# Performance work log

Hardware: AMD Instinct MI355X
Metric: run time of the kernel (lower is better)

## Reference

```python
import jax, jax.numpy as jnp
import numpy as np

D_MODEL = 1024
NUM_HEADS = 16
HEAD_DIM = D_MODEL // NUM_HEADS


def setup_inputs() -> dict:
    key = jax.random.key(0)
    ks = jax.random.split(key, 9)
    B, S = 4, 2048
    s = 1.0 / np.sqrt(D_MODEL)
    return {
        "x": jax.random.normal(ks[0], (B, S, D_MODEL), dtype=jnp.float32),
        "Wq": jax.random.normal(ks[1], (D_MODEL, D_MODEL), dtype=jnp.float32) * s,
        "bq": jnp.zeros((D_MODEL,), dtype=jnp.float32),
        "Wk": jax.random.normal(ks[2], (D_MODEL, HEAD_DIM), dtype=jnp.float32) * s,
        "bk": jnp.zeros((HEAD_DIM,), dtype=jnp.float32),
        "Wv": jax.random.normal(ks[3], (D_MODEL, HEAD_DIM), dtype=jnp.float32) * s,
        "bv": jnp.zeros((HEAD_DIM,), dtype=jnp.float32),
        "Wo": jax.random.normal(ks[4], (D_MODEL, D_MODEL), dtype=jnp.float32) * s,
        "bo": jnp.zeros((D_MODEL,), dtype=jnp.float32),
    }


def reference(x, Wq, bq, Wk, bk, Wv, bv, Wo, bo):
    B, S, _ = x.shape
    H, Dh = NUM_HEADS, HEAD_DIM
    # projections
    Q = (x @ Wq + bq).reshape(B, S, H, Dh).transpose(0, 2, 1, 3)  # [B,H,S,Dh]
    K = x @ Wk + bk  # [B,S,Dh] (single shared KV head)
    V = x @ Wv + bv  # [B,S,Dh]
    # scores: Q @ K^T, broadcasting the single K head over all query heads
    A = jnp.einsum("bhqd,bkd->bhqk", Q, K)  # [B,H,S,S]
    causal = jnp.tril(jnp.ones((S, S), dtype=bool))
    A = jnp.where(causal, A, -jnp.inf)
    # original divides AFTER masking; -inf stays -inf so math is identical
    P = jax.nn.softmax(A / np.sqrt(Dh).astype(np.float32), axis=-1)
    O = jnp.einsum("bhqk,bkd->bhqd", P, V)  # [B,H,S,Dh]
    O = O.transpose(0, 2, 1, 3).reshape(B, S, H * Dh)
    return O @ Wo + bo
```

## Files before the change

kernel.cpp:

```cpp
#include <hip/hip_runtime.h>
#include <hip/hip_bf16.h>

typedef __bf16 bf16_t;
typedef __bf16 bf16x4 __attribute__((ext_vector_type(4)));
typedef __bf16 bf16x8 __attribute__((ext_vector_type(8)));
typedef float f32x4 __attribute__((ext_vector_type(4)));

#define AS1(p) ((const __attribute__((address_space(1))) void*)(p))
#define AS3(p) ((__attribute__((address_space(3))) void*)(p))

__device__ __forceinline__ f32x4 mfma16(bf16x8 a, bf16x8 b, f32x4 c) {
  return __builtin_amdgcn_mfma_f32_16x16x32_bf16(a, b, c, 0, 0, 0);
}

__global__ void cvt_f32_to_bf16(const float* __restrict__ in, bf16_t* __restrict__ out, int n) {
  int i = (blockIdx.x * 256 + threadIdx.x) * 4;
  if (i >= n) return;
  float4 v = *(const float4*)(in + i);
  bf16x4 o = {(bf16_t)v.x, (bf16_t)v.y, (bf16_t)v.z, (bf16_t)v.w};
  *(bf16x4*)(out + i) = o;
}

__global__ void transpose_cvt_t(const float* __restrict__ W, bf16_t* __restrict__ Wt,
                                int K, int N) {
  __shared__ float t[64][65];
  const int n0 = blockIdx.x * 64, k0 = blockIdx.y * 64;
  const int tx = threadIdx.x & 63, ty = threadIdx.x >> 6;
#pragma unroll
  for (int i = 0; i < 16; ++i)
    t[ty * 16 + i][tx] = W[(size_t)(k0 + ty * 16 + i) * N + n0 + tx];
  __syncthreads();
#pragma unroll
  for (int i = 0; i < 16; ++i)
    Wt[(size_t)(n0 + ty * 16 + i) * K + k0 + tx] = (bf16_t)t[tx][ty * 16 + i];
}

__global__ void transpose_v(const bf16_t* __restrict__ Vb, bf16_t* __restrict__ VtG) {
  __shared__ bf16_t t[64][72];
  const int s0 = blockIdx.x * 64, b = blockIdx.y;
  const int tx = threadIdx.x & 63, ty = threadIdx.x >> 6;
#pragma unroll
  for (int i = 0; i < 16; ++i)
    t[ty * 16 + i][tx] = Vb[(size_t)(b * 2048 + s0 + ty * 16 + i) * 64 + tx];
  __syncthreads();
#pragma unroll
  for (int i = 0; i < 16; ++i)
    VtG[(size_t)(b * 64 + ty * 16 + i) * 2048 + s0 + tx] = t[tx][ty * 16 + i];
}

__global__ __launch_bounds__(256, 2)
void gemm_nt_bias_b16(const bf16_t* __restrict__ A, const bf16_t* __restrict__ Bt,
                      const float* __restrict__ bias, bf16_t* __restrict__ C,
                      int M, int N, int K) {
  __shared__ __align__(16) bf16_t As[128 * 32];
  __shared__ __align__(16) bf16_t Bs[128 * 32];
  const int tid = threadIdx.x;
  const int w = tid >> 6, l = tid & 63;
  const int l15 = l & 15, q = l >> 4;
  const int m0 = blockIdx.x * 128, n0 = blockIdx.y * 128;
  const int mw = (w >> 1) * 64, nw = (w & 1) * 64;
  f32x4 acc[4][4] = {};
  const int kb = (l & 3) * 8;
  int rA[2], rB[2];
#pragma unroll
  for (int i = 0; i < 2; ++i) {
    int row = (i * 4 + w) * 16 + (l >> 2);
    rA[i] = m0 + row;
    int rb = n0 + row; if (rb >= N) rb = N - 1;
    rB[i] = rb;
  }
  for (int k0 = 0; k0 < K; k0 += 32) {
#pragma unroll
    for (int i = 0; i < 2; ++i) {
      int sg = i * 4 + w;
      __builtin_amdgcn_global_load_lds(AS1(A + (size_t)rA[i] * K + k0 + kb),
                                       AS3(As + sg * 512), 16, 0, 0);
      __builtin_amdgcn_global_load_lds(AS1(Bt + (size_t)rB[i] * K + k0 + kb),
                                       AS3(Bs + sg * 512), 16, 0, 0);
    }
    __syncthreads();
    bf16x8 af[4], bfr[4];
#pragma unroll
    for (int mi = 0; mi < 4; ++mi)
      af[mi] = *(const bf16x8*)(As + (mw + mi * 16 + l15) * 32 + q * 8);
#pragma unroll
    for (int ni = 0; ni < 4; ++ni)
      bfr[ni] = *(const bf16x8*)(Bs + (nw + ni * 16 + l15) * 32 + q * 8);
#pragma unroll
    for (int mi = 0; mi < 4; ++mi)
#pragma unroll
      for (int ni = 0; ni < 4; ++ni)
        acc[mi][ni] = mfma16(af[mi], bfr[ni], acc[mi][ni]);
    __syncthreads();
  }
#pragma unroll
  for (int ni = 0; ni < 4; ++ni) {
    int col = n0 + nw + ni * 16 + l15;
    if (col >= N) continue;
    float bv = bias[col];
#pragma unroll
    for (int mi = 0; mi < 4; ++mi)
#pragma unroll
      for (int r = 0; r < 4; ++r) {
        int row = m0 + mw + mi * 16 + q * 4 + r;
        C[(size_t)row * N + col] = (bf16_t)(acc[mi][ni][r] + bv);
      }
  }
}

__global__ __launch_bounds__(256, 2)
void gemm_nt_bias_f32(const bf16_t* __restrict__ A, const bf16_t* __restrict__ Bt,
                      const float* __restrict__ bias, float* __restrict__ C,
                      int M, int N, int K) {
  __shared__ __align__(16) bf16_t As[128 * 32];
  __shared__ __align__(16) bf16_t Bs[128 * 32];
  const int tid = threadIdx.x;
  const int w = tid >> 6, l = tid & 63;
  const int l15 = l & 15, q = l >> 4;
  const int m0 = blockIdx.x * 128, n0 = blockIdx.y * 128;
  const int mw = (w >> 1) * 64, nw = (w & 1) * 64;
  f32x4 acc[4][4] = {};
  const int kb = (l & 3) * 8;
  int rA[2], rB[2];
#pragma unroll
  for (int i = 0; i < 2; ++i) {
    int row = (i * 4 + w) * 16 + (l >> 2);
    rA[i] = m0 + row;
    int rb = n0 + row; if (rb >= N) rb = N - 1;
    rB[i] = rb;
  }
  for (int k0 = 0; k0 < K; k0 += 32) {
#pragma unroll
    for (int i = 0; i < 2; ++i) {
      int sg = i * 4 + w;
      __builtin_amdgcn_global_load_lds(AS1(A + (size_t)rA[i] * K + k0 + kb),
                                       AS3(As + sg * 512), 16, 0, 0);
      __builtin_amdgcn_global_load_lds(AS1(Bt + (size_t)rB[i] * K + k0 + kb),
                                       AS3(Bs + sg * 512), 16, 0, 0);
    }
    __syncthreads();
    bf16x8 af[4], bfr[4];
#pragma unroll
    for (int mi = 0; mi < 4; ++mi)
      af[mi] = *(const bf16x8*)(As + (mw + mi * 16 + l15) * 32 + q * 8);
#pragma unroll
    for (int ni = 0; ni < 4; ++ni)
      bfr[ni] = *(const bf16x8*)(Bs + (nw + ni * 16 + l15) * 32 + q * 8);
#pragma unroll
    for (int mi = 0; mi < 4; ++mi)
#pragma unroll
      for (int ni = 0; ni < 4; ++ni)
        acc[mi][ni] = mfma16(af[mi], bfr[ni], acc[mi][ni]);
    __syncthreads();
  }
#pragma unroll
  for (int ni = 0; ni < 4; ++ni) {
    int col = n0 + nw + ni * 16 + l15;
    if (col >= N) continue;
    float bv = bias[col];
#pragma unroll
    for (int mi = 0; mi < 4; ++mi)
#pragma unroll
      for (int r = 0; r < 4; ++r) {
        int row = m0 + mw + mi * 16 + q * 4 + r;
        C[(size_t)row * N + col] = acc[mi][ni][r] + bv;
      }
  }
}

__device__ __forceinline__ void attn_range(
    const bf16_t* __restrict__ Qb, const bf16_t* __restrict__ kbase,
    const bf16_t* __restrict__ vbase, int b, int h, int qt, int kt0, int kt1,
    int l15, int q, bf16_t* __restrict__ ps, f32x4 (&o)[4][4], float (&rs)[4]) {
  bf16x8 qf0[4], qf1[4];
#pragma unroll
  for (int nq = 0; nq < 4; ++nq) {
    const bf16_t* qp = Qb + (size_t)(b * 2048 + qt * 64 + nq * 16 + l15) * 1024 + h * 64 + q * 8;
    qf0[nq] = *(const bf16x8*)qp;
    qf1[nq] = *(const bf16x8*)(qp + 32);
  }
  const float c1 = 0.18033688f;
  for (int kt = kt0; kt < kt1; ++kt) {
    const bf16_t* kb = kbase + (size_t)kt * 64 * 64;
    bf16x8 ka0[4], ka1[4];
#pragma unroll
    for (int mk = 0; mk < 4; ++mk) {
      const bf16_t* kr = kb + (mk * 16 + l15) * 64;
      ka0[mk] = *(const bf16x8*)(kr + q * 8);
      ka1[mk] = *(const bf16x8*)(kr + 32 + q * 8);
    }
    bf16x8 va0[4], va1[4];
#pragma unroll
    for (int md = 0; md < 4; ++md) {
      const bf16_t* vr = vbase + (size_t)(md * 16 + l15) * 2048 + kt * 64;
      va0[md] = *(const bf16x8*)(vr + q * 8);
      va1[md] = *(const bf16x8*)(vr + 32 + q * 8);
    }
    const bool diag = (kt == qt);
#pragma unroll
    for (int mh = 0; mh < 2; ++mh) {
      f32x4 s2[2][4];
      __builtin_amdgcn_s_setprio(1);
#pragma unroll
      for (int mk2 = 0; mk2 < 2; ++mk2)
#pragma unroll
        for (int nq = 0; nq < 4; ++nq) {
          f32x4 t = {0.f, 0.f, 0.f, 0.f};
          t = mfma16(ka0[mh * 2 + mk2], qf0[nq], t);
          t = mfma16(ka1[mh * 2 + mk2], qf1[nq], t);
          s2[mk2][nq] = t;
        }
      __builtin_amdgcn_s_setprio(0);
#pragma unroll
      for (int nq = 0; nq < 4; ++nq)
#pragma unroll
        for (int mk2 = 0; mk2 < 2; ++mk2) {
          const int mk = mh * 2 + mk2;
          bf16x4 pk;
#pragma unroll
          for (int r = 0; r < 4; ++r) {
            float pv = __builtin_amdgcn_exp2f(s2[mk2][nq][r] * c1 - 16.0f);
            if (diag && (mk * 16 + q * 4 + r) > (nq * 16 + l15)) pv = 0.f;
            rs[nq] += pv;
            pk[r] = (bf16_t)pv;
          }
          *(bf16x4*)(ps + nq * 1152 + l15 * 72 + mk * 16 + q * 4) = pk;
        }
    }
#pragma unroll
    for (int nq = 0; nq < 4; ++nq) {
      bf16x8 pb0 = *(const bf16x8*)(ps + nq * 1152 + l15 * 72 + q * 8);
      bf16x8 pb1 = *(const bf16x8*)(ps + nq * 1152 + l15 * 72 + 32 + q * 8);
      __builtin_amdgcn_s_setprio(1);
#pragma unroll
      for (int md = 0; md < 4; ++md) {
        o[md][nq] = mfma16(va0[md], pb0, o[md][nq]);
        o[md][nq] = mfma16(va1[md], pb1, o[md][nq]);
      }
      __builtin_amdgcn_s_setprio(0);
    }
  }
}

__device__ __forceinline__ void attn_finalize(bf16_t* __restrict__ AO, int b, int h,
                                              int qt, int l15, int q,
                                              f32x4 (&o)[4][4], float (&rs)[4]) {
#pragma unroll
  for (int nq = 0; nq < 4; ++nq) {
    rs[nq] += __shfl_xor(rs[nq], 16);
    rs[nq] += __shfl_xor(rs[nq], 32);
  }
  float inv[4];
#pragma unroll
  for (int nq = 0; nq < 4; ++nq) inv[nq] = 1.f / rs[nq];
#pragma unroll
  for (int md = 0; md < 4; ++md)
#pragma unroll
    for (int nq = 0; nq < 4; ++nq) {
      bf16x4 ov = {(bf16_t)(o[md][nq][0] * inv[nq]), (bf16_t)(o[md][nq][1] * inv[nq]),
                   (bf16_t)(o[md][nq][2] * inv[nq]), (bf16_t)(o[md][nq][3] * inv[nq])};
      *(bf16x4*)(AO + (size_t)(b * 2048 + qt * 64 + nq * 16 + l15) * 1024 +
                 h * 64 + md * 16 + q * 4) = ov;
    }
}

__global__ __launch_bounds__(128, 2)
void mqa_attn6(const bf16_t* __restrict__ Qb, const bf16_t* __restrict__ Kb,
               const bf16_t* __restrict__ VtG, bf16_t* __restrict__ AO) {
  __shared__ __align__(16) bf16_t Ps[2][4][16 * 72];
  __shared__ __align__(16) float Oc[4096];
  __shared__ float RSc[256];
  const int u = blockIdx.x;
  const int b = u & 3;
  const int h = (u >> 2) & 15;
  const int p = (u >> 6) & 15;
  const int w = threadIdx.x >> 6, l = threadIdx.x & 63;
  const int l15 = l & 15, q = l >> 4;
  const int qt_h = 31 - p;
  bf16_t* ps = &Ps[w][0][0];
  const bf16_t* kbase = Kb + (size_t)b * 2048 * 64;
  const bf16_t* vbase = VtG + (size_t)b * 64 * 2048;

  f32x4 o[4][4] = {};
  float rs[4] = {0.f, 0.f, 0.f, 0.f};

  if (w == 0) {
    attn_range(Qb, kbase, vbase, b, h, qt_h, 0, 17, l15, q, ps, o, rs);
    __syncthreads();
#pragma unroll
    for (int md = 0; md < 4; ++md)
#pragma unroll
      for (int nq = 0; nq < 4; ++nq)
        o[md][nq] += *(const f32x4*)&Oc[((md * 4 + nq) * 64 + l) * 4];
#pragma unroll
    for (int nq = 0; nq < 4; ++nq) rs[nq] += RSc[l * 4 + nq];
    attn_finalize(AO, b, h, qt_h, l15, q, o, rs);
  } else {
    attn_range(Qb, kbase, vbase, b, h, p, 0, p + 1, l15, q, ps, o, rs);
    attn_finalize(AO, b, h, p, l15, q, o, rs);
#pragma unroll
    for (int md = 0; md < 4; ++md)
#pragma unroll
      for (int nq = 0; nq < 4; ++nq) o[md][nq] = f32x4{0.f, 0.f, 0.f, 0.f};
    rs[0] = rs[1] = rs[2] = rs[3] = 0.f;
    attn_range(Qb, kbase, vbase, b, h, qt_h, 17, 32 - p, l15, q, ps, o, rs);
#pragma unroll
    for (int md = 0; md < 4; ++md)
#pragma unroll
      for (int nq = 0; nq < 4; ++nq)
        *(f32x4*)&Oc[((md * 4 + nq) * 64 + l) * 4] = o[md][nq];
#pragma unroll
    for (int nq = 0; nq < 4; ++nq) RSc[l * 4 + nq] = rs[nq];
    __syncthreads();
  }
}

extern "C" void kernel_launch(void* const* d_in, const int* in_sizes, int n_in,
                              void* d_out, int out_size, void* d_ws, size_t ws_size,
                              hipStream_t stream) {
  (void)in_sizes; (void)n_in; (void)out_size; (void)ws_size;
  const int BS = 8192;
  const float* x  = (const float*)d_in[0];
  const float* Wq = (const float*)d_in[1];
  const float* bq = (const float*)d_in[2];
  const float* Wk = (const float*)d_in[3];
  const float* bk = (const float*)d_in[4];
  const float* Wv = (const float*)d_in[5];
  const float* bv = (const float*)d_in[6];
  const float* Wo = (const float*)d_in[7];
  const float* bo = (const float*)d_in[8];
  float* out = (float*)d_out;

  bf16_t* p = (bf16_t*)d_ws;
  bf16_t* WqT = p; p += 1024 * 1024;
  bf16_t* WkT = p; p += 64 * 1024;
  bf16_t* WvT = p; p += 64 * 1024;
  bf16_t* WoT = p; p += 1024 * 1024;
  bf16_t* xb  = p; p += (size_t)BS * 1024;
  bf16_t* Qb  = p; p += (size_t)BS * 1024;
  bf16_t* Kb  = p; p += (size_t)BS * 64;
  bf16_t* Vb  = p; p += (size_t)BS * 64;
  bf16_t* AO  = xb;
  bf16_t* VtG = WqT;

  cvt_f32_to_bf16<<<(BS * 1024 / 4 + 255) / 256, 256, 0, stream>>>(x, xb, BS * 1024);
  transpose_cvt_t<<<dim3(16, 16), 256, 0, stream>>>(Wq, WqT, 1024, 1024);
  transpose_cvt_t<<<dim3(1, 16), 256, 0, stream>>>(Wk, WkT, 1024, 64);
  transpose_cvt_t<<<dim3(1, 16), 256, 0, stream>>>(Wv, WvT, 1024, 64);
  transpose_cvt_t<<<dim3(16, 16), 256, 0, stream>>>(Wo, WoT, 1024, 1024);

  gemm_nt_bias_b16<<<dim3(BS / 128, 8), 256, 0, stream>>>(xb, WqT, bq, Qb, BS, 1024, 1024);
  gemm_nt_bias_b16<<<dim3(BS / 128, 1), 256, 0, stream>>>(xb, WkT, bk, Kb, BS, 64, 1024);
  gemm_nt_bias_b16<<<dim3(BS / 128, 1), 256, 0, stream>>>(xb, WvT, bv, Vb, BS, 64, 1024);

  transpose_v<<<dim3(32, 4), 256, 0, stream>>>(Vb, VtG);

  mqa_attn6<<<dim3(1024), 128, 0, stream>>>(Qb, Kb, VtG, AO);

  gemm_nt_bias_f32<<<dim3(BS / 128, 8), 256, 0, stream>>>(AO, WoT, bo, out, BS, 1024, 1024);
}
```

Measured before the change: 277.1 us.

## Fuse prep kernels, merge K/V GEMM with V transpose, template diagonal masking

Folds the x conversion, four weight transposes and a K/V bias concat into one prep launch. The separate K and V projections become a single N=128 GEMM that also writes V transposed directly, removing the transpose_v kernel. The attention loop is split into a templated step so only the diagonal tile pays for the causal mask check. The goal is fewer launches, less intermediate traffic and less per-tile branching, at the cost of scattered 2-byte transposed stores in the GEMM epilogue and a wider KV stride in the attention loads.

```diff
diff --git a/kernel.cpp b/kernel.cpp
--- a/kernel.cpp
+++ b/kernel.cpp
@@ -13,18 +13,32 @@
   return __builtin_amdgcn_mfma_f32_16x16x32_bf16(a, b, c, 0, 0, 0);
 }
 
-__global__ void cvt_f32_to_bf16(const float* __restrict__ in, bf16_t* __restrict__ out, int n) {
-  int i = (blockIdx.x * 256 + threadIdx.x) * 4;
-  if (i >= n) return;
-  float4 v = *(const float4*)(in + i);
-  bf16x4 o = {(bf16_t)v.x, (bf16_t)v.y, (bf16_t)v.z, (bf16_t)v.w};
-  *(bf16x4*)(out + i) = o;
-}
-
-__global__ void transpose_cvt_t(const float* __restrict__ W, bf16_t* __restrict__ Wt,
-                                int K, int N) {
+__global__ void prep(const float* __restrict__ x, const float* __restrict__ Wq,
+                     const float* __restrict__ Wk, const float* __restrict__ Wv,
+                     const float* __restrict__ Wo, const float* __restrict__ bk,
+                     const float* __restrict__ bv, bf16_t* __restrict__ xb,
+                     bf16_t* __restrict__ WqT, bf16_t* __restrict__ WkvT,
+                     bf16_t* __restrict__ WoT, float* __restrict__ bkv) {
+  const int u = blockIdx.x;
+  if (u >= 545) {
+    int i = ((u - 545) * 256 + threadIdx.x) * 4;
+    float4 v = *(const float4*)(x + i);
+    bf16x4 o = {(bf16_t)v.x, (bf16_t)v.y, (bf16_t)v.z, (bf16_t)v.w};
+    *(bf16x4*)(xb + i) = o;
+    return;
+  }
+  if (u == 544) {
+    if (threadIdx.x < 128)
+      bkv[threadIdx.x] = (threadIdx.x < 64) ? bk[threadIdx.x] : bv[threadIdx.x - 64];
+    return;
+  }
+  const float* W; bf16_t* Wt; int N, bx, by;
+  if (u < 256)      { W = Wq; Wt = WqT;             N = 1024; bx = u & 15;        by = u >> 4; }
+  else if (u < 272) { W = Wk; Wt = WkvT;            N = 64;   bx = 0;             by = u - 256; }
+  else if (u < 288) { W = Wv; Wt = WkvT + 64 * 1024; N = 64;  bx = 0;             by = u - 272; }
+  else              { W = Wo; Wt = WoT;             N = 1024; bx = (u - 288) & 15; by = (u - 288) >> 4; }
   __shared__ float t[64][65];
-  const int n0 = blockIdx.x * 64, k0 = blockIdx.y * 64;
+  const int n0 = bx * 64, k0 = by * 64;
   const int tx = threadIdx.x & 63, ty = threadIdx.x >> 6;
 #pragma unroll
   for (int i = 0; i < 16; ++i)
@@ -32,20 +46,7 @@
   __syncthreads();
 #pragma unroll
   for (int i = 0; i < 16; ++i)
-    Wt[(size_t)(n0 + ty * 16 + i) * K + k0 + tx] = (bf16_t)t[tx][ty * 16 + i];
-}
-
-__global__ void transpose_v(const bf16_t* __restrict__ Vb, bf16_t* __restrict__ VtG) {
-  __shared__ bf16_t t[64][72];
-  const int s0 = blockIdx.x * 64, b = blockIdx.y;
-  const int tx = threadIdx.x & 63, ty = threadIdx.x >> 6;
-#pragma unroll
-  for (int i = 0; i < 16; ++i)
-    t[ty * 16 + i][tx] = Vb[(size_t)(b * 2048 + s0 + ty * 16 + i) * 64 + tx];
-  __syncthreads();
-#pragma unroll
-  for (int i = 0; i < 16; ++i)
-    VtG[(size_t)(b * 64 + ty * 16 + i) * 2048 + s0 + tx] = t[tx][ty * 16 + i];
+    Wt[(size_t)(n0 + ty * 16 + i) * 1024 + k0 + tx] = (bf16_t)t[tx][ty * 16 + i];
 }
 
 __global__ __launch_bounds__(256, 2)
@@ -109,6 +110,67 @@
 }
 
 __global__ __launch_bounds__(256, 2)
+void gemm_kv(const bf16_t* __restrict__ A, const bf16_t* __restrict__ Bt,
+             const float* __restrict__ bias, bf16_t* __restrict__ C,
+             bf16_t* __restrict__ VtG, int M, int K) {
+  __shared__ __align__(16) bf16_t As[128 * 32];
+  __shared__ __align__(16) bf16_t Bs[128 * 32];
+  const int tid = threadIdx.x;
+  const int w = tid >> 6, l = tid & 63;
+  const int l15 = l & 15, q = l >> 4;
+  const int m0 = blockIdx.x * 128;
+  const int mw = (w >> 1) * 64, nw = (w & 1) * 64;
+  f32x4 acc[4][4] = {};
+  const int kb = (l & 3) * 8;
+  int rA[2], rB[2];
+#pragma unroll
+  for (int i = 0; i < 2; ++i) {
+    int row = (i * 4 + w) * 16 + (l >> 2);
+    rA[i] = m0 + row;
+    rB[i] = row;
+  }
+  for (int k0 = 0; k0 < K; k0 += 32) {
+#pragma unroll
+    for (int i = 0; i < 2; ++i) {
+      int sg = i * 4 + w;
+      __builtin_amdgcn_global_load_lds(AS1(A + (size_t)rA[i] * K + k0 + kb),
+                                       AS3(As + sg * 512), 16, 0, 0);
+      __builtin_amdgcn_global_load_lds(AS1(Bt + (size_t)rB[i] * K + k0 + kb),
+                                       AS3(Bs + sg * 512), 16, 0, 0);
+    }
+    __syncthreads();
+    bf16x8 af[4], bfr[4];
+#pragma unroll
+    for (int mi = 0; mi < 4; ++mi)
+      af[mi] = *(const bf16x8*)(As + (mw + mi * 16 + l15) * 32 + q * 8);
+#pragma unroll
+    for (int ni = 0; ni < 4; ++ni)
+      bfr[ni] = *(const bf16x8*)(Bs + (nw + ni * 16 + l15) * 32 + q * 8);
+#pragma unroll
+    for (int mi = 0; mi < 4; ++mi)
+#pragma unroll
+      for (int ni = 0; ni < 4; ++ni)
+        acc[mi][ni] = mfma16(af[mi], bfr[ni], acc[mi][ni]);
+    __syncthreads();
+  }
+#pragma unroll
+  for (int ni = 0; ni < 4; ++ni) {
+    int col = nw + ni * 16 + l15;
+    float bv = bias[col];
+#pragma unroll
+    for (int mi = 0; mi < 4; ++mi)
+#pragma unroll
+      for (int r = 0; r < 4; ++r) {
+        int row = m0 + mw + mi * 16 + q * 4 + r;
+        bf16_t v = (bf16_t)(acc[mi][ni][r] + bv);
+        C[(size_t)row * 128 + col] = v;
+        if (col >= 64)
+          VtG[(size_t)((row >> 11) * 64 + (col - 64)) * 2048 + (row & 2047)] = v;
+      }
+  }
+}
+
+__global__ __launch_bounds__(256, 2)
 void gemm_nt_bias_f32(const bf16_t* __restrict__ A, const bf16_t* __restrict__ Bt,
                       const float* __restrict__ bias, float* __restrict__ C,
                       int M, int N, int K) {
@@ -168,77 +230,80 @@
   }
 }
 
-__device__ __forceinline__ void attn_range(
-    const bf16_t* __restrict__ Qb, const bf16_t* __restrict__ kbase,
-    const bf16_t* __restrict__ vbase, int b, int h, int qt, int kt0, int kt1,
-    int l15, int q, bf16_t* __restrict__ ps, f32x4 (&o)[4][4], float (&rs)[4]) {
-  bf16x8 qf0[4], qf1[4];
+__device__ __forceinline__ void load_q(const bf16_t* __restrict__ Qb, int b, int h,
+                                       int qt, int l15, int q,
+                                       bf16x8 (&qf0)[4], bf16x8 (&qf1)[4]) {
 #pragma unroll
   for (int nq = 0; nq < 4; ++nq) {
     const bf16_t* qp = Qb + (size_t)(b * 2048 + qt * 64 + nq * 16 + l15) * 1024 + h * 64 + q * 8;
     qf0[nq] = *(const bf16x8*)qp;
     qf1[nq] = *(const bf16x8*)(qp + 32);
   }
+}
+
+template <bool DIAG>
+__device__ __forceinline__ void attn_step(
+    const bf16_t* __restrict__ kbase, const bf16_t* __restrict__ vbase, int kt,
+    int l15, int q, bf16_t* __restrict__ ps,
+    const bf16x8 (&qf0)[4], const bf16x8 (&qf1)[4],
+    f32x4 (&o)[4][4], float (&rs)[4]) {
   const float c1 = 0.18033688f;
-  for (int kt = kt0; kt < kt1; ++kt) {
-    const bf16_t* kb = kbase + (size_t)kt * 64 * 64;
-    bf16x8 ka0[4], ka1[4];
-#pragma unroll
-    for (int mk = 0; mk < 4; ++mk) {
-      const bf16_t* kr = kb + (mk * 16 + l15) * 64;
-      ka0[mk] = *(const bf16x8*)(kr + q * 8);
-      ka1[mk] = *(const bf16x8*)(kr + 32 + q * 8);
-    }
-    bf16x8 va0[4], va1[4];
+  const bf16_t* kb = kbase + (size_t)kt * 64 * 128;
+  bf16x8 ka0[4], ka1[4];
+#pragma unroll
+  for (int mk = 0; mk < 4; ++mk) {
+    const bf16_t* kr = kb + (mk * 16 + l15) * 128;
+    ka0[mk] = *(const bf16x8*)(kr + q * 8);
+    ka1[mk] = *(const bf16x8*)(kr + 32 + q * 8);
+  }
+  bf16x8 va0[4], va1[4];
+#pragma unroll
+  for (int md = 0; md < 4; ++md) {
+    const bf16_t* vr = vbase + (size_t)(md * 16 + l15) * 2048 + kt * 64;
+    va0[md] = *(const bf16x8*)(vr + q * 8);
+    va1[md] = *(const bf16x8*)(vr + 32 + q * 8);
+  }
+#pragma unroll
+  for (int mh = 0; mh < 2; ++mh) {
+    f32x4 s2[2][4];
+    __builtin_amdgcn_s_setprio(1);
+#pragma unroll
+    for (int mk2 = 0; mk2 < 2; ++mk2)
+#pragma unroll
+      for (int nq = 0; nq < 4; ++nq) {
+        f32x4 t = {0.f, 0.f, 0.f, 0.f};
+        t = mfma16(ka0[mh * 2 + mk2], qf0[nq], t);
+        t = mfma16(ka1[mh * 2 + mk2], qf1[nq], t);
+        s2[mk2][nq] = t;
+      }
+    __builtin_amdgcn_s_setprio(0);
+#pragma unroll
+    for (int nq = 0; nq < 4; ++nq)
+#pragma unroll
+      for (int mk2 = 0; mk2 < 2; ++mk2) {
+        const int mk = mh * 2 + mk2;
+        bf16x4 pk;
+#pragma unroll
+        for (int r = 0; r < 4; ++r) {
+          float pv = __builtin_amdgcn_exp2f(s2[mk2][nq][r] * c1 - 16.0f);
+          if (DIAG && (mk * 16 + q * 4 + r) > (nq * 16 + l15)) pv = 0.f;
+          rs[nq] += pv;
+          pk[r] = (bf16_t)pv;
+        }
+        *(bf16x4*)(ps + nq * 1152 + l15 * 72 + mk * 16 + q * 4) = pk;
+      }
+  }
+#pragma unroll
+  for (int nq = 0; nq < 4; ++nq) {
+    bf16x8 pb0 = *(const bf16x8*)(ps + nq * 1152 + l15 * 72 + q * 8);
+    bf16x8 pb1 = *(const bf16x8*)(ps + nq * 1152 + l15 * 72 + 32 + q * 8);
+    __builtin_amdgcn_s_setprio(1);
 #pragma unroll
     for (int md = 0; md < 4; ++md) {
-      const bf16_t* vr = vbase + (size_t)(md * 16 + l15) * 2048 + kt * 64;
-      va0[md] = *(const bf16x8*)(vr + q * 8);
-      va1[md] = *(const bf16x8*)(vr + 32 + q * 8);
-    }
-    const bool diag = (kt == qt);
-#pragma unroll
-    for (int mh = 0; mh < 2; ++mh) {
-      f32x4 s2[2][4];
-      __builtin_amdgcn_s_setprio(1);
-#pragma unroll
-      for (int mk2 = 0; mk2 < 2; ++mk2)
-#pragma unroll
-        for (int nq = 0; nq < 4; ++nq) {
-          f32x4 t = {0.f, 0.f, 0.f, 0.f};
-          t = mfma16(ka0[mh * 2 + mk2], qf0[nq], t);
-          t = mfma16(ka1[mh * 2 + mk2], qf1[nq], t);
-          s2[mk2][nq] = t;
-        }
-      __builtin_amdgcn_s_setprio(0);
-#pragma unroll
-      for (int nq = 0; nq < 4; ++nq)
-#pragma unroll
-        for (int mk2 = 0; mk2 < 2; ++mk2) {
-          const int mk = mh * 2 + mk2;
-          bf16x4 pk;
-#pragma unroll
-          for (int r = 0; r < 4; ++r) {
-            float pv = __builtin_amdgcn_exp2f(s2[mk2][nq][r] * c1 - 16.0f);
-            if (diag && (mk * 16 + q * 4 + r) > (nq * 16 + l15)) pv = 0.f;
-            rs[nq] += pv;
-            pk[r] = (bf16_t)pv;
-          }
-          *(bf16x4*)(ps + nq * 1152 + l15 * 72 + mk * 16 + q * 4) = pk;
-        }
-    }
-#pragma unroll
-    for (int nq = 0; nq < 4; ++nq) {
-      bf16x8 pb0 = *(const bf16x8*)(ps + nq * 1152 + l15 * 72 + q * 8);
-      bf16x8 pb1 = *(const bf16x8*)(ps + nq * 1152 + l15 * 72 + 32 + q * 8);
-      __builtin_amdgcn_s_setprio(1);
-#pragma unroll
-      for (int md = 0; md < 4; ++md) {
-        o[md][nq] = mfma16(va0[md], pb0, o[md][nq]);
-        o[md][nq] = mfma16(va1[md], pb1, o[md][nq]);
-      }
-      __builtin_amdgcn_s_setprio(0);
-    }
+      o[md][nq] = mfma16(va0[md], pb0, o[md][nq]);
+      o[md][nq] = mfma16(va1[md], pb1, o[md][nq]);
+    }
+    __builtin_amdgcn_s_setprio(0);
   }
 }
 
@@ -265,7 +330,7 @@
 }
 
 __global__ __launch_bounds__(128, 2)
-void mqa_attn6(const bf16_t* __restrict__ Qb, const bf16_t* __restrict__ Kb,
+void mqa_attn9(const bf16_t* __restrict__ Qb, const bf16_t* __restrict__ KVb,
                const bf16_t* __restrict__ VtG, bf16_t* __restrict__ AO) {
   __shared__ __align__(16) bf16_t Ps[2][4][16 * 72];
   __shared__ __align__(16) float Oc[4096];
@@ -278,14 +343,20 @@
   const int l15 = l & 15, q = l >> 4;
   const int qt_h = 31 - p;
   bf16_t* ps = &Ps[w][0][0];
-  const bf16_t* kbase = Kb + (size_t)b * 2048 * 64;
+  const bf16_t* kbase = KVb + (size_t)b * 2048 * 128;
   const bf16_t* vbase = VtG + (size_t)b * 64 * 2048;
 
+  bf16x8 qf0[4], qf1[4];
   f32x4 o[4][4] = {};
   float rs[4] = {0.f, 0.f, 0.f, 0.f};
 
   if (w == 0) {
-    attn_range(Qb, kbase, vbase, b, h, qt_h, 0, 17, l15, q, ps, o, rs);
+    load_q(Qb, b, h, qt_h, l15, q, qf0, qf1);
+    const int e = (p == 15) ? 16 : 17;
+    for (int kt = 0; kt < e; ++kt)
+      attn_step<false>(kbase, vbase, kt, l15, q, ps, qf0, qf1, o, rs);
+    if (p == 15)
+      attn_step<true>(kbase, vbase, 16, l15, q, ps, qf0, qf1, o, rs);
     __syncthreads();
 #pragma unroll
     for (int md = 0; md < 4; ++md)
@@ -296,14 +367,22 @@
     for (int nq = 0; nq < 4; ++nq) rs[nq] += RSc[l * 4 + nq];
     attn_finalize(AO, b, h, qt_h, l15, q, o, rs);
   } else {
-    attn_range(Qb, kbase, vbase, b, h, p, 0, p + 1, l15, q, ps, o, rs);
+    load_q(Qb, b, h, p, l15, q, qf0, qf1);
+    for (int kt = 0; kt < p; ++kt)
+      attn_step<false>(kbase, vbase, kt, l15, q, ps, qf0, qf1, o, rs);
+    attn_step<true>(kbase, vbase, p, l15, q, ps, qf0, qf1, o, rs);
     attn_finalize(AO, b, h, p, l15, q, o, rs);
 #pragma unroll
     for (int md = 0; md < 4; ++md)
 #pragma unroll
       for (int nq = 0; nq < 4; ++nq) o[md][nq] = f32x4{0.f, 0.f, 0.f, 0.f};
     rs[0] = rs[1] = rs[2] = rs[3] = 0.f;
-    attn_range(Qb, kbase, vbase, b, h, qt_h, 17, 32 - p, l15, q, ps, o, rs);
+    if (p < 15) {
+      load_q(Qb, b, h, qt_h, l15, q, qf0, qf1);
+      for (int kt = 17; kt < 31 - p; ++kt)
+        attn_step<false>(kbase, vbase, kt, l15, q, ps, qf0, qf1, o, rs);
+      attn_step<true>(kbase, vbase, 31 - p, l15, q, ps, qf0, qf1, o, rs);
+    }
 #pragma unroll
     for (int md = 0; md < 4; ++md)
 #pragma unroll
@@ -332,30 +411,23 @@
   float* out = (float*)d_out;
 
   bf16_t* p = (bf16_t*)d_ws;
-  bf16_t* WqT = p; p += 1024 * 1024;
-  bf16_t* WkT = p; p += 64 * 1024;
-  bf16_t* WvT = p; p += 64 * 1024;
-  bf16_t* WoT = p; p += 1024 * 1024;
-  bf16_t* xb  = p; p += (size_t)BS * 1024;
-  bf16_t* Qb  = p; p += (size_t)BS * 1024;
-  bf16_t* Kb  = p; p += (size_t)BS * 64;
-  bf16_t* Vb  = p; p += (size_t)BS * 64;
+  bf16_t* WqT  = p; p += 1024 * 1024;
+  bf16_t* WkvT = p; p += 128 * 1024;
+  bf16_t* WoT  = p; p += 1024 * 1024;
+  bf16_t* xb   = p; p += (size_t)BS * 1024;
+  bf16_t* Qb   = p; p += (size_t)BS * 1024;
+  bf16_t* KVb  = p; p += (size_t)BS * 128;
+  float*  bkv  = (float*)p; p += 256;
   bf16_t* AO  = xb;
   bf16_t* VtG = WqT;
 
-  cvt_f32_to_bf16<<<(BS * 1024 / 4 + 255) / 256, 256, 0, stream>>>(x, xb, BS * 1024);
-  transpose_cvt_t<<<dim3(16, 16), 256, 0, stream>>>(Wq, WqT, 1024, 1024);
-  transpose_cvt_t<<<dim3(1, 16), 256, 0, stream>>>(Wk, WkT, 1024, 64);
-  transpose_cvt_t<<<dim3(1, 16), 256, 0, stream>>>(Wv, WvT, 1024, 64);
-  transpose_cvt_t<<<dim3(16, 16), 256, 0, stream>>>(Wo, WoT, 1024, 1024);
+  prep<<<dim3(545 + BS * 1024 / 1024), 256, 0, stream>>>(
+      x, Wq, Wk, Wv, Wo, bk, bv, xb, WqT, WkvT, WoT, bkv);
 
   gemm_nt_bias_b16<<<dim3(BS / 128, 8), 256, 0, stream>>>(xb, WqT, bq, Qb, BS, 1024, 1024);
-  gemm_nt_bias_b16<<<dim3(BS / 128, 1), 256, 0, stream>>>(xb, WkT, bk, Kb, BS, 64, 1024);
-  gemm_nt_bias_b16<<<dim3(BS / 128, 1), 256, 0, stream>>>(xb, WvT, bv, Vb, BS, 64, 1024);
-
-  transpose_v<<<dim3(32, 4), 256, 0, stream>>>(Vb, VtG);
-
-  mqa_attn6<<<dim3(1024), 128, 0, stream>>>(Qb, Kb, VtG, AO);
+  gemm_kv<<<dim3(BS / 128, 1), 256, 0, stream>>>(xb, WkvT, bkv, KVb, VtG, BS, 1024);
+
+  mqa_attn9<<<dim3(1024), 128, 0, stream>>>(Qb, KVb, VtG, AO);
 
   gemm_nt_bias_f32<<<dim3(BS / 128, 8), 256, 0, stream>>>(AO, WoT, bo, out, BS, 1024, 1024);
 }
```

Measured after the change: 247.9 us. -10.6%, faster.
